# Kernel tuning notes

Measured on AMD Instinct MI355X. Metric: run time of the kernel, lower is better.

## Reference

```python
import jax, jax.numpy as jnp
import numpy as np

B, H, V, MAX_MSG_LEN = 8192, 512, 512, 16


def _uniform(key, shape, scale):
    return jax.random.uniform(key, shape, jnp.float32, -scale, scale)


def setup_inputs() -> dict:
    key = jax.random.key(0)
    ks = jax.random.split(key, 9)
    s = 1.0 / np.sqrt(H)  # torch LSTMCell/Linear default init scale
    return {
        "encoder_hidden": jax.random.normal(ks[0], (B, H), jnp.float32),
        "encoder_cell": jax.random.normal(ks[1], (B, H), jnp.float32),
        "W_ih": _uniform(ks[2], (4 * H, V), s),   # LSTMCell input weights (i,f,g,o)
        "W_hh": _uniform(ks[3], (4 * H, H), s),   # LSTMCell hidden weights
        "b_ih": _uniform(ks[4], (4 * H,), s),
        "b_hh": _uniform(ks[5], (4 * H,), s),
        "W_out": _uniform(ks[6], (V, H), s),      # nn.Linear(hidden, io_size)
        "b_out": _uniform(ks[7], (V,), s),
        "init_input": jnp.zeros((1, V), jnp.float32),  # nn.Parameter zeros
    }


def reference(encoder_hidden, encoder_cell, W_ih, W_hh, b_ih, b_hh, W_out, b_out, init_input):
    batch = encoder_hidden.shape[0]
    x0 = jnp.broadcast_to(init_input, (batch, init_input.shape[1]))

    def step(carry, _):
        x, h, c, m, lp = carry
        # torch LSTMCell: gates ordered (i, f, g, o)
        gates = x @ W_ih.T + b_ih + h @ W_hh.T + b_hh
        i, f, g, o = jnp.split(gates, 4, axis=-1)
        c = jax.nn.sigmoid(f) * c + jax.nn.sigmoid(i) * jnp.tanh(g)
        h = jax.nn.sigmoid(o) * jnp.tanh(c)
        probs = jax.nn.softmax(h @ W_out.T + b_out, axis=1)  # [B, V]
        # eval path: one-hot of argmax
        predict = jax.nn.one_hot(jnp.argmax(probs, axis=1), probs.shape[1], dtype=probs.dtype)
        lp = lp + jnp.log((probs * predict).sum(axis=1)) * m
        new_m = m * (1.0 - predict[:, -1])  # last vocab index acts as EOS
        return (predict, h, c, new_m, lp), (predict, m)

    carry0 = (x0, encoder_hidden, encoder_cell,
              jnp.ones((batch,), jnp.float32), jnp.zeros((batch,), jnp.float32))
    (_, _, _, _, log_probs), (message, masks) = jax.lax.scan(step, carry0, None, length=MAX_MSG_LEN)
    # message: [L, B, V]; mask stacked as [L, 1, B] like torch.stack of [1, B] rows
    return message, masks[:, None, :], log_probs
```

## Files before the change

kernel.cpp:

```cpp
#include <hip/hip_runtime.h>
#include <math.h>

#define Bsz 8192
#define Hd  512
#define Vd  512
#define Ld  16
#define G4  2048
#define NSLAB 16

using int4v  = __attribute__((ext_vector_type(4))) int;

__device__ __forceinline__ float sigm_f(float x){
  return __builtin_amdgcn_rcpf(1.0f + __expf(-x));
}
__device__ __forceinline__ float tanh_f(float x){
  return 1.0f - 2.0f * __builtin_amdgcn_rcpf(1.0f + __expf(2.0f * x));
}

__device__ __forceinline__ void i16split(float x, float S, signed char& a, signed char& b){
  int q = (int)rintf(x * S);
  q = min(max(q, -32640), 32639);
  const int ah = (q + 128) >> 8;
  a = (signed char)ah;
  b = (signed char)(q - (ah << 8));
}

__device__ __forceinline__ void gl_lds16(const void* g, void* l){
  __builtin_amdgcn_global_load_lds((const __attribute__((address_space(1))) void*)g,
                                   (__attribute__((address_space(3))) void*)l, 16, 0, 0);
}

#define PHASE_SYNC(N) asm volatile("s_waitcnt vmcnt(" #N ")\n\ts_barrier" ::: "memory")
#define LDS_SYNC() asm volatile("s_waitcnt lgkmcnt(0)\n\ts_barrier" ::: "memory")

#define C1I (65536.0f / (524288.0f * 32767.0f))
#define C2I (  256.0f / (524288.0f * 32767.0f))
#define C1E (65536.0f / (524288.0f * 4096.0f))
#define C2E (  256.0f / (524288.0f * 4096.0f))

#define MFMA3Q(g,bt) \
  acc1[g][bt] = __builtin_amdgcn_mfma_i32_16x16x64_i8(wA[g], hf[bt], acc1[g][bt], 0,0,0); \
  acc2[g][bt] = __builtin_amdgcn_mfma_i32_16x16x64_i8(wA[g], lf[bt], acc2[g][bt], 0,0,0); \
  acc2[g][bt] = __builtin_amdgcn_mfma_i32_16x16x64_i8(wB[g], hf[bt], acc2[g][bt], 0,0,0);

__device__ __forceinline__ int xcd_tau(int nwg_div8){
  const int lin  = blockIdx.y * gridDim.x + blockIdx.x;
  const int xcd  = lin & 7;
  const int slot = lin >> 3;
  return xcd * nwg_div8 + slot;
}

__global__ __launch_bounds__(256) void k_transpose(const float* __restrict__ in,
                                                   float* __restrict__ out){
  __shared__ float tile[32][33];
  const int tx = threadIdx.x, ty = threadIdx.y;
  const int v0 = blockIdx.x * 32, n0 = blockIdx.y * 32;
#pragma unroll
  for(int i=0;i<4;i++)
    tile[ty+i*8][tx] = in[(size_t)(n0+ty+i*8)*Vd + v0+tx];
  __syncthreads();
#pragma unroll
  for(int i=0;i<4;i++)
    out[(size_t)(v0+ty+i*8)*G4 + n0+tx] = tile[tx][ty+i*8];
}

__global__ __launch_bounds__(256) void k_split_i8(const float* __restrict__ src,
                                                  signed char* __restrict__ pa,
                                                  signed char* __restrict__ pb,
                                                  float S, int n){
  const int i = blockIdx.x*256 + threadIdx.x;
  if(i < n){
    signed char a, b;
    i16split(src[i], S, a, b);
    pa[i] = a; pb[i] = b;
  }
}

template<bool FIRST>
__global__ __launch_bounds__(512, 2) void k_lstm8(
    const signed char* __restrict__ hA, const signed char* __restrict__ hB,
    const float* __restrict__ cin,
    signed char* __restrict__ hoA, signed char* __restrict__ hoB,
    float* __restrict__ cout,
    const signed char* __restrict__ WA, const signed char* __restrict__ WB,
    const float* __restrict__ WihT, const float* __restrict__ bih,
    const float* __restrict__ bhh,
    const float* __restrict__ statM, const float* __restrict__ statS,
    const int* __restrict__ statI,
    float* __restrict__ msg, float* __restrict__ masks_out,
    float* __restrict__ lp_out, float* __restrict__ lpbuf,
    float* __restrict__ mbuf, int prev)
{
  __shared__ unsigned char lds[2][49152];
  __shared__ int gIs[256];
  const int tid = threadIdx.x;
  const int wave = tid >> 6, lane = tid & 63;
  const int tau = xcd_tau(64);
  const int mb = (tau >> 4) * 256;
  const int jb = (tau & 15) * 32;
  const int wjj = wave >> 2;
  const int wbb = wave & 3;
  const int j_wave = wjj * 16;
  const int b_wave = wbb * 64;
  const int fr = lane & 15, q = lane >> 4;
  const int lr = lane >> 2, jj = lane & 3;

  auto stW = [&](int k0, int bsel){
    unsigned char* Wa = lds[bsel];
    unsigned char* Wb = lds[bsel] + 8192;
    const int s = wave;
    const int r = s*16 + lr;
    const int j = jj ^ ((r >> 1) & 3);
    const size_t ka = (size_t)k0 + j*16;
    const size_t wrow = (size_t)((r >> 5)*Hd + jb + (r & 31));
    gl_lds16(WA + wrow*Hd + ka, &Wa[s*1024]);
    gl_lds16(WB + wrow*Hd + ka, &Wb[s*1024]);
  };
  auto stH = [&](int k0, int bsel, int half){
    unsigned char* Ha = lds[bsel] + 16384;
    unsigned char* Hb = lds[bsel] + 32768;
    const int s = (wave >> 1)*4 + half*2 + (wave & 1);
    const int r = s*16 + lr;
    const int j = jj ^ ((r >> 1) & 3);
    const size_t ka = (size_t)k0 + j*16;
    gl_lds16(hA + (size_t)(mb + r)*Hd + ka, &Ha[s*1024]);
    gl_lds16(hB + (size_t)(mb + r)*Hd + ka, &Hb[s*1024]);
  };

  stW(0, 0); stH(0, 0, 0); stH(0, 0, 1);

  int xid[4] = {0,0,0,0};
  if(!FIRST){
    if(tid < 256){
      const int row = mb + tid;
      float gm = statM[row]; int gi = statI[row];
#pragma unroll
      for(int s=1;s<NSLAB;s++){
        const float m = statM[(size_t)s*Bsz + row];
        if(m > gm){ gm = m; gi = statI[(size_t)s*Bsz + row]; }
      }
      if(jb == 0){
        float tot = 0.0f;
#pragma unroll
        for(int s=0;s<NSLAB;s++)
          tot += statS[(size_t)s*Bsz + row] * __expf(statM[(size_t)s*Bsz + row] - gm);
        const float logp = -__logf(tot);
        const float mo  = (prev == 0) ? 1.0f : mbuf[row];
        const float lpo = (prev == 0) ? 0.0f : lpbuf[row];
        const float lpn = lpo + logp * mo;
        masks_out[(size_t)prev * Bsz + row] = mo;
        lp_out[row] = lpn;
        lpbuf[row]  = lpn;
        mbuf[row]   = mo * ((gi == Vd-1) ? 0.0f : 1.0f);
      }
      gIs[tid] = gi;
    }
    LDS_SYNC();

    {
      const int r  = tid >> 1;
      const int c0 = jb + (tid & 1) * 16;
      const int gi = gIs[r];
      float* mrow = msg + ((size_t)prev * Bsz + mb + r) * Vd;
#pragma unroll
      for(int i=0;i<4;i++){
        const int c = c0 + i*4;
        float4 v;
        v.x = (c   == gi) ? 1.0f : 0.0f;
        v.y = (c+1 == gi) ? 1.0f : 0.0f;
        v.z = (c+2 == gi) ? 1.0f : 0.0f;
        v.w = (c+3 == gi) ? 1.0f : 0.0f;
        *(float4*)&mrow[c] = v;
      }
    }
#pragma unroll
    for(int bt=0;bt<4;bt++)
      xid[bt] = gIs[b_wave + bt*16 + fr];
  }

  int4v acc1[4][4], acc2[4][4];
#pragma unroll
  for(int g=0;g<4;g++)
#pragma unroll
    for(int bt=0;bt<4;bt++){
      acc1[g][bt] = (int4v){0,0,0,0};
      acc2[g][bt] = (int4v){0,0,0,0};
    }

  int4v wA[4], wB[4], hf[4], lf[4];
  for(int t=0; t<8; t++){
    const int cur = t & 1, nxt = cur ^ 1;
    const int kn = ((t+1) & 7) * 64;
    const unsigned char* Wa = lds[cur];
    const unsigned char* Wb = lds[cur] + 8192;
    const unsigned char* Ha = lds[cur] + 16384;
    const unsigned char* Hb = lds[cur] + 32768;

    PHASE_SYNC(2);
#pragma unroll
    for(int g=0;g<2;g++){
      const int r = g*32 + j_wave + fr;
      const int off = r*64 + ((q ^ ((r >> 1) & 3)) << 4);
      wA[g] = *(const int4v*)&Wa[off];
      wB[g] = *(const int4v*)&Wb[off];
    }
#pragma unroll
    for(int bt=0;bt<2;bt++){
      const int r = b_wave + bt*16 + fr;
      const int off = r*64 + ((q ^ ((r >> 1) & 3)) << 4);
      hf[bt] = *(const int4v*)&Ha[off];
      lf[bt] = *(const int4v*)&Hb[off];
    }
    stW(kn, nxt);
    __builtin_amdgcn_s_setprio(1);
#pragma unroll
    for(int g=0;g<2;g++)
#pragma unroll
      for(int bt=0;bt<2;bt++){ MFMA3Q(g,bt) }
    __builtin_amdgcn_s_setprio(0);

#pragma unroll
    for(int g=2;g<4;g++){
      const int r = g*32 + j_wave + fr;
      const int off = r*64 + ((q ^ ((r >> 1) & 3)) << 4);
      wA[g] = *(const int4v*)&Wa[off];
      wB[g] = *(const int4v*)&Wb[off];
    }
    stH(kn, nxt, 0);
    __builtin_amdgcn_s_setprio(1);
#pragma unroll
    for(int g=2;g<4;g++)
#pragma unroll
      for(int bt=0;bt<2;bt++){ MFMA3Q(g,bt) }
    __builtin_amdgcn_s_setprio(0);

    PHASE_SYNC(4);
#pragma unroll
    for(int bt=2;bt<4;bt++){
      const int r = b_wave + bt*16 + fr;
      const int off = r*64 + ((q ^ ((r >> 1) & 3)) << 4);
      hf[bt] = *(const int4v*)&Ha[off];
      lf[bt] = *(const int4v*)&Hb[off];
    }
    stH(kn, nxt, 1);
    __builtin_amdgcn_s_setprio(1);
#pragma unroll
    for(int g=0;g<2;g++)
#pragma unroll
      for(int bt=2;bt<4;bt++){ MFMA3Q(g,bt) }
    __builtin_amdgcn_s_setprio(0);

    __builtin_amdgcn_s_setprio(1);
#pragma unroll
    for(int g=2;g<4;g++)
#pragma unroll
      for(int bt=2;bt<4;bt++){ MFMA3Q(g,bt) }
    __builtin_amdgcn_s_setprio(0);
  }

  const float c1 = FIRST ? C1E : C1I;
  const float c2 = FIRST ? C2E : C2I;
  const int j0 = jb + j_wave + q*4;
  float bsum[4][4];
#pragma unroll
  for(int g=0;g<4;g++){
    float4 a = *(const float4*)&bih[g*Hd + j0];
    float4 b = *(const float4*)&bhh[g*Hd + j0];
    bsum[g][0]=a.x+b.x; bsum[g][1]=a.y+b.y; bsum[g][2]=a.z+b.z; bsum[g][3]=a.w+b.w;
  }
#pragma unroll
  for(int bt=0;bt<4;bt++){
    const int b = mb + b_wave + bt*16 + fr;
    const size_t idx = (size_t)b*Hd + j0;
    float gv[4][4];
#pragma unroll
    for(int g=0;g<4;g++)
#pragma unroll
      for(int r=0;r<4;r++)
        gv[g][r] = fmaf(c1, (float)acc1[g][bt][r],
                   fmaf(c2, (float)acc2[g][bt][r], bsum[g][r]));
    if(!FIRST){
      const float* grow = WihT + (size_t)xid[bt]*G4 + j0;
#pragma unroll
      for(int g=0;g<4;g++){
        float4 x = *(const float4*)&grow[g*Hd];
        gv[g][0]+=x.x; gv[g][1]+=x.y; gv[g][2]+=x.z; gv[g][3]+=x.w;
      }
    }
    float co[4];
    *(float4*)co = *(const float4*)&cin[idx];
    float cn[4];
    signed char a4[4], b4[4];
#pragma unroll
    for(int r=0;r<4;r++){
      const float I = sigm_f(gv[0][r]);
      const float F = sigm_f(gv[1][r]);
      const float G = tanh_f(gv[2][r]);
      const float O = sigm_f(gv[3][r]);
      cn[r] = F*co[r] + I*G;
      const float hn = O*tanh_f(cn[r]);
      i16split(hn, 32767.0f, a4[r], b4[r]);
    }
    *(float4*)&cout[idx] = *(float4*)cn;
    *(char4*)&hoA[idx] = *(char4*)a4;
    *(char4*)&hoB[idx] = *(char4*)b4;
  }
}

__global__ __launch_bounds__(512, 2) void k_logits8(
    const signed char* __restrict__ hA, const signed char* __restrict__ hB,
    const signed char* __restrict__ WoA, const signed char* __restrict__ WoB,
    const float* __restrict__ bout,
    float* __restrict__ statM, float* __restrict__ statS, int* __restrict__ statI)
{
  __shared__ unsigned char lds[2][40960];
  const int tid = threadIdx.x;
  const int wave = tid >> 6, lane = tid & 63;
  const int tau = xcd_tau(32);
  const int mb = (tau >> 3) * 256;
  const int vb = (tau & 7) * 64;
  const int wv = wave >> 2;
  const int wm = wave & 3;
  const int n_wave = wv * 32;
  const int m_wave = wm * 64;
  const int fr = lane & 15, q = lane >> 4;
  const int lr = lane >> 2, jj = lane & 3;

  auto stA = [&](int k0, int bsel){
    unsigned char* Ha = lds[bsel];
    unsigned char* Hb = lds[bsel] + 16384;
    unsigned char* Wp = lds[bsel] + 32768;
    {
      const int s = (wave >> 1)*4 + (wave & 1);
      const int r = s*16 + lr;
      const int j = jj ^ ((r >> 1) & 3);
      const size_t ka = (size_t)k0 + j*16;
      gl_lds16(hA + (size_t)(mb + r)*Hd + ka, &Ha[s*1024]);
      gl_lds16(hB + (size_t)(mb + r)*Hd + ka, &Hb[s*1024]);
    }
    {
      const int pl = wave >> 2;
      const int s  = wave & 3;
      const int r = s*16 + lr;
      const int j = jj ^ ((r >> 1) & 3);
      const size_t ka = (size_t)k0 + j*16;
      const signed char* src = pl ? WoB : WoA;
      gl_lds16(src + (size_t)(vb + r)*Hd + ka, &Wp[pl*4096 + s*1024]);
    }
  };
  auto stB = [&](int k0, int bsel){
    unsigned char* Ha = lds[bsel];
    unsigned char* Hb = lds[bsel] + 16384;
    const int s = (wave >> 1)*4 + 2 + (wave & 1);
    const int r = s*16 + lr;
    const int j = jj ^ ((r >> 1) & 3);
    const size_t ka = (size_t)k0 + j*16;
    gl_lds16(hA + (size_t)(mb + r)*Hd + ka, &Ha[s*1024]);
    gl_lds16(hB + (size_t)(mb + r)*Hd + ka, &Hb[s*1024]);
  };

  stA(0, 0); stB(0, 0);

  int4v acc1[2][4], acc2[2][4];
#pragma unroll
  for(int nt=0;nt<2;nt++)
#pragma unroll
    for(int mt=0;mt<4;mt++){
      acc1[nt][mt] = (int4v){0,0,0,0};
      acc2[nt][mt] = (int4v){0,0,0,0};
    }

  int4v ah[4], al[4], bh[2], bl[2];
  for(int t=0; t<8; t++){
    const int cur = t & 1, nxt = cur ^ 1;
    const int kn = ((t+1) & 7) * 64;
    const unsigned char* Ha = lds[cur];
    const unsigned char* Hb = lds[cur] + 16384;
    const unsigned char* Wa = lds[cur] + 32768;
    const unsigned char* Wb = lds[cur] + 36864;

    PHASE_SYNC(2);
#pragma unroll
    for(int nt=0;nt<2;nt++){
      const int r = n_wave + nt*16 + fr;
      const int off = r*64 + ((q ^ ((r >> 1) & 3)) << 4);
      bh[nt] = *(const int4v*)&Wa[off];
      bl[nt] = *(const int4v*)&Wb[off];
    }
#pragma unroll
    for(int mt=0;mt<2;mt++){
      const int r = m_wave + mt*16 + fr;
      const int off = r*64 + ((q ^ ((r >> 1) & 3)) << 4);
      ah[mt] = *(const int4v*)&Ha[off];
      al[mt] = *(const int4v*)&Hb[off];
    }
    stA(kn, nxt);
    __builtin_amdgcn_s_setprio(1);
#pragma unroll
    for(int nt=0;nt<2;nt++)
#pragma unroll
      for(int mt=0;mt<2;mt++){
        acc1[nt][mt] = __builtin_amdgcn_mfma_i32_16x16x64_i8(ah[mt], bh[nt], acc1[nt][mt], 0,0,0);
        acc2[nt][mt] = __builtin_amdgcn_mfma_i32_16x16x64_i8(ah[mt], bl[nt], acc2[nt][mt], 0,0,0);
        acc2[nt][mt] = __builtin_amdgcn_mfma_i32_16x16x64_i8(al[mt], bh[nt], acc2[nt][mt], 0,0,0);
      }
    __builtin_amdgcn_s_setprio(0);

    PHASE_SYNC(3);
#pragma unroll
    for(int mt=2;mt<4;mt++){
      const int r = m_wave + mt*16 + fr;
      const int off = r*64 + ((q ^ ((r >> 1) & 3)) << 4);
      ah[mt] = *(const int4v*)&Ha[off];
      al[mt] = *(const int4v*)&Hb[off];
    }
    stB(kn, nxt);
    __builtin_amdgcn_s_setprio(1);
#pragma unroll
    for(int nt=0;nt<2;nt++)
#pragma unroll
      for(int mt=2;mt<4;mt++){
        acc1[nt][mt] = __builtin_amdgcn_mfma_i32_16x16x64_i8(ah[mt], bh[nt], acc1[nt][mt], 0,0,0);
        acc2[nt][mt] = __builtin_amdgcn_mfma_i32_16x16x64_i8(ah[mt], bl[nt], acc2[nt][mt], 0,0,0);
        acc2[nt][mt] = __builtin_amdgcn_mfma_i32_16x16x64_i8(al[mt], bh[nt], acc2[nt][mt], 0,0,0);
      }
    __builtin_amdgcn_s_setprio(0);
  }

  const int slab = (vb >> 5) + wv;
  float bo[2];
  int vv[2];
#pragma unroll
  for(int nt=0;nt<2;nt++){
    vv[nt] = vb + n_wave + nt*16 + fr;
    bo[nt] = bout[vv[nt]];
  }
#pragma unroll
  for(int mt=0;mt<4;mt++){
#pragma unroll
    for(int reg=0;reg<4;reg++){
      float lg[2];
#pragma unroll
      for(int nt=0;nt<2;nt++)
        lg[nt] = fmaf(C1I, (float)acc1[nt][mt][reg],
                 fmaf(C2I, (float)acc2[nt][mt][reg], bo[nt]));
      float vmax = lg[0];
      int   imax = vv[0];
      if(lg[1] > vmax || (lg[1] == vmax && vv[1] < imax)){ vmax = lg[1]; imax = vv[1]; }
#pragma unroll
      for(int off=1; off<16; off<<=1){
        const float vo = __shfl_xor(vmax, off);
        const int   io = __shfl_xor(imax, off);
        if(vo > vmax || (vo == vmax && io < imax)){ vmax = vo; imax = io; }
      }
      float s = __expf(lg[0] - vmax) + __expf(lg[1] - vmax);
#pragma unroll
      for(int off=1; off<16; off<<=1) s += __shfl_xor(s, off);
      if(fr == 0){
        const int m = mb + m_wave + mt*16 + q*4 + reg;
        statM[(size_t)slab*Bsz + m] = vmax;
        statS[(size_t)slab*Bsz + m] = s;
        statI[(size_t)slab*Bsz + m] = imax;
      }
    }
  }
}

__global__ __launch_bounds__(256) void k_merge(
    const float* __restrict__ statM, const float* __restrict__ statS,
    const int* __restrict__ statI,
    float* __restrict__ msg, float* __restrict__ masks_out,
    float* __restrict__ lp_out, float* __restrict__ lpbuf,
    float* __restrict__ mbuf, int step)
{
  __shared__ int gI[32];
  const int tid = threadIdx.x;
  const int mb = blockIdx.x * 32;

  if(tid < 32){
    const int row = mb + tid;
    float gm = statM[row]; int gi = statI[row];
#pragma unroll
    for(int s=1;s<NSLAB;s++){
      const float m = statM[(size_t)s*Bsz + row];
      if(m > gm){ gm = m; gi = statI[(size_t)s*Bsz + row]; }
    }
    float tot = 0.0f;
#pragma unroll
    for(int s=0;s<NSLAB;s++)
      tot += statS[(size_t)s*Bsz + row] * __expf(statM[(size_t)s*Bsz + row] - gm);
    const float logp = -__logf(tot);
    const float mo  = mbuf[row];
    const float lpn = lpbuf[row] + logp * mo;
    masks_out[(size_t)step * Bsz + row] = mo;
    lp_out[row] = lpn;
    gI[tid] = gi;
  }
  __syncthreads();

  const int r  = tid >> 3;
  const int c8 = tid & 7;
  const int gi = gI[r];
  float* mrow = msg + ((size_t)step * Bsz + mb + r) * Vd;
#pragma unroll
  for(int i=0;i<16;i++){
    const int c = (i*8 + c8) * 4;
    float4 v;
    v.x = (c   == gi) ? 1.0f : 0.0f;
    v.y = (c+1 == gi) ? 1.0f : 0.0f;
    v.z = (c+2 == gi) ? 1.0f : 0.0f;
    v.w = (c+3 == gi) ? 1.0f : 0.0f;
    *(float4*)&mrow[c] = v;
  }
}

extern "C" void kernel_launch(void* const* d_in, const int* in_sizes, int n_in,
                              void* d_out, int out_size, void* d_ws, size_t ws_size,
                              hipStream_t stream) {
  const float* enc_h = (const float*)d_in[0];
  const float* enc_c = (const float*)d_in[1];
  const float* Wih   = (const float*)d_in[2];
  const float* Whh   = (const float*)d_in[3];
  const float* bih   = (const float*)d_in[4];
  const float* bhh   = (const float*)d_in[5];
  const float* Wout  = (const float*)d_in[6];
  const float* bout  = (const float*)d_in[7];

  float* out_msg   = (float*)d_out;
  float* out_masks = out_msg + (size_t)Ld * Bsz * Vd;
  float* out_lp    = out_masks + (size_t)Ld * Bsz;

  char* ws = (char*)d_ws;
  float* WihT  = (float*)ws;          ws += (size_t)Vd * G4 * 4;
  signed char* WhhA = (signed char*)ws; ws += (size_t)G4 * Hd;
  signed char* WhhB = (signed char*)ws; ws += (size_t)G4 * Hd;
  signed char* WoA  = (signed char*)ws; ws += (size_t)Vd * Hd;
  signed char* WoB  = (signed char*)ws; ws += (size_t)Vd * Hd;
  signed char* encA = (signed char*)ws; ws += (size_t)Bsz * Hd;
  signed char* encB = (signed char*)ws; ws += (size_t)Bsz * Hd;
  signed char* ha0  = (signed char*)ws; ws += (size_t)Bsz * Hd;
  signed char* hb0  = (signed char*)ws; ws += (size_t)Bsz * Hd;
  signed char* ha1  = (signed char*)ws; ws += (size_t)Bsz * Hd;
  signed char* hb1  = (signed char*)ws; ws += (size_t)Bsz * Hd;
  float* cbuf   = (float*)ws;  ws += (size_t)Bsz * Hd * 4;
  float* statM  = (float*)ws;  ws += (size_t)NSLAB * Bsz * 4;
  float* statS  = (float*)ws;  ws += (size_t)NSLAB * Bsz * 4;
  int*   statI  = (int*)ws;    ws += (size_t)NSLAB * Bsz * 4;
  float* lpbuf  = (float*)ws;  ws += (size_t)Bsz * 4;
  float* mbuf   = (float*)ws;  ws += (size_t)Bsz * 4;

  k_transpose<<<dim3(Vd/32, G4/32), dim3(32,8), 0, stream>>>(Wih, WihT);
  k_split_i8<<<(G4*Hd+255)/256, 256, 0, stream>>>(Whh, WhhA, WhhB, 524288.0f, G4*Hd);
  k_split_i8<<<(Vd*Hd+255)/256, 256, 0, stream>>>(Wout, WoA, WoB, 524288.0f, Vd*Hd);
  k_split_i8<<<(Bsz*Hd+255)/256, 256, 0, stream>>>(enc_h, encA, encB, 4096.0f, Bsz*Hd);

  for(int t=0; t<Ld; t++){
    signed char* haOut = (t & 1) ? ha1 : ha0;
    signed char* hbOut = (t & 1) ? hb1 : hb0;
    const signed char* haIn = (t & 1) ? ha0 : ha1;
    const signed char* hbIn = (t & 1) ? hb0 : hb1;

    if(t == 0){
      k_lstm8<true><<<dim3(Bsz/256, Hd/32), 512, 0, stream>>>(
          encA, encB, enc_c, haOut, hbOut, cbuf, WhhA, WhhB, WihT, bih, bhh,
          nullptr, nullptr, nullptr, nullptr, nullptr, nullptr, nullptr, nullptr, 0);
    } else {
      k_lstm8<false><<<dim3(Bsz/256, Hd/32), 512, 0, stream>>>(
          haIn, hbIn, cbuf, haOut, hbOut, cbuf, WhhA, WhhB, WihT, bih, bhh,
          statM, statS, statI, out_msg, out_masks, out_lp, lpbuf, mbuf, t-1);
    }
    k_logits8<<<dim3(Bsz/256, Vd/64), 512, 0, stream>>>(
        haOut, hbOut, WoA, WoB, bout, statM, statS, statI);
  }
  k_merge<<<Bsz/32, 256, 0, stream>>>(statM, statS, statI,
                                      out_msg, out_masks, out_lp,
                                      lpbuf, mbuf, Ld-1);
}
```

Before: 1.235 ms.

## Fuse LSTM step, output logits and argmax merge into one per-step kernel

Replaces the separate LSTM-gate, logits and merge kernels with a single kernel per timestep. Each block owns 32 batch rows and loops over all gate-weight chunks and then all output-weight chunks, keeping the new hidden state in LDS so the logits GEMM reads it directly. Softmax stats and argmax are reduced inside the block, which removes the slab statistics buffers and the extra launches. Gate weights and biases are interleaved per hidden unit and the cell state is stored transposed. The cost is that every block streams the full weight matrices, so weight traffic rises sharply and batch-tile reuse is much lower than the previous 256-row tiles.

```diff
diff --git a/kernel.cpp b/kernel.cpp
--- a/kernel.cpp
+++ b/kernel.cpp
@@ -6,9 +6,9 @@
 #define Vd  512
 #define Ld  16
 #define G4  2048
-#define NSLAB 16
-
-using int4v  = __attribute__((ext_vector_type(4))) int;
+#define BM  32
+
+using int4v = __attribute__((ext_vector_type(4))) int;
 
 __device__ __forceinline__ float sigm_f(float x){
   return __builtin_amdgcn_rcpf(1.0f + __expf(-x));
@@ -30,28 +30,13 @@
                                    (__attribute__((address_space(3))) void*)l, 16, 0, 0);
 }
 
-#define PHASE_SYNC(N) asm volatile("s_waitcnt vmcnt(" #N ")\n\ts_barrier" ::: "memory")
-#define LDS_SYNC() asm volatile("s_waitcnt lgkmcnt(0)\n\ts_barrier" ::: "memory")
-
 #define C1I (65536.0f / (524288.0f * 32767.0f))
 #define C2I (  256.0f / (524288.0f * 32767.0f))
 #define C1E (65536.0f / (524288.0f * 4096.0f))
 #define C2E (  256.0f / (524288.0f * 4096.0f))
 
-#define MFMA3Q(g,bt) \
-  acc1[g][bt] = __builtin_amdgcn_mfma_i32_16x16x64_i8(wA[g], hf[bt], acc1[g][bt], 0,0,0); \
-  acc2[g][bt] = __builtin_amdgcn_mfma_i32_16x16x64_i8(wA[g], lf[bt], acc2[g][bt], 0,0,0); \
-  acc2[g][bt] = __builtin_amdgcn_mfma_i32_16x16x64_i8(wB[g], hf[bt], acc2[g][bt], 0,0,0);
-
-__device__ __forceinline__ int xcd_tau(int nwg_div8){
-  const int lin  = blockIdx.y * gridDim.x + blockIdx.x;
-  const int xcd  = lin & 7;
-  const int slot = lin >> 3;
-  return xcd * nwg_div8 + slot;
-}
-
-__global__ __launch_bounds__(256) void k_transpose(const float* __restrict__ in,
-                                                   float* __restrict__ out){
+__global__ __launch_bounds__(256) void k_prep_wih(const float* __restrict__ in,
+                                                  float* __restrict__ out){
   __shared__ float tile[32][33];
   const int tx = threadIdx.x, ty = threadIdx.y;
   const int v0 = blockIdx.x * 32, n0 = blockIdx.y * 32;
@@ -59,9 +44,38 @@
   for(int i=0;i<4;i++)
     tile[ty+i*8][tx] = in[(size_t)(n0+ty+i*8)*Vd + v0+tx];
   __syncthreads();
+  const int g = n0 >> 9, jb = n0 & 511;
 #pragma unroll
   for(int i=0;i<4;i++)
-    out[(size_t)(v0+ty+i*8)*G4 + n0+tx] = tile[tx][ty+i*8];
+    out[(size_t)(v0+ty+i*8)*G4 + (jb+tx)*4 + g] = tile[tx][ty+i*8];
+}
+
+__global__ __launch_bounds__(256) void k_tr_c(const float* __restrict__ in,
+                                              float* __restrict__ out){
+  __shared__ float tile[32][33];
+  const int tx = threadIdx.x, ty = threadIdx.y;
+  const int j0 = blockIdx.x * 32, b0 = blockIdx.y * 32;
+#pragma unroll
+  for(int i=0;i<4;i++)
+    tile[ty+i*8][tx] = in[(size_t)(b0+ty+i*8)*Hd + j0+tx];
+  __syncthreads();
+#pragma unroll
+  for(int i=0;i<4;i++)
+    out[(size_t)(j0+ty+i*8)*Bsz + b0+tx] = tile[tx][ty+i*8];
+}
+
+__global__ __launch_bounds__(256) void k_split_whh(const float* __restrict__ src,
+                                                   signed char* __restrict__ pa,
+                                                   signed char* __restrict__ pb){
+  const int i = blockIdx.x*256 + threadIdx.x;
+  if(i < G4*Hd){
+    const int in_row = i >> 9, k = i & 511;
+    const int o_row = (in_row & 511)*4 + (in_row >> 9);
+    signed char a, b;
+    i16split(src[i], 524288.0f, a, b);
+    pa[(size_t)o_row*Hd + k] = a;
+    pb[(size_t)o_row*Hd + k] = b;
+  }
 }
 
 __global__ __launch_bounds__(256) void k_split_i8(const float* __restrict__ src,
@@ -76,441 +90,260 @@
   }
 }
 
+__global__ __launch_bounds__(256) void k_prep_bias(const float* __restrict__ bih,
+                                                   const float* __restrict__ bhh,
+                                                   float* __restrict__ out){
+  const int i = blockIdx.x*256 + threadIdx.x;
+  if(i < G4)
+    out[(i & 511)*4 + (i >> 9)] = bih[i] + bhh[i];
+}
+
 template<bool FIRST>
-__global__ __launch_bounds__(512, 2) void k_lstm8(
-    const signed char* __restrict__ hA, const signed char* __restrict__ hB,
-    const float* __restrict__ cin,
-    signed char* __restrict__ hoA, signed char* __restrict__ hoB,
-    float* __restrict__ cout,
-    const signed char* __restrict__ WA, const signed char* __restrict__ WB,
-    const float* __restrict__ WihT, const float* __restrict__ bih,
-    const float* __restrict__ bhh,
-    const float* __restrict__ statM, const float* __restrict__ statS,
-    const int* __restrict__ statI,
-    float* __restrict__ msg, float* __restrict__ masks_out,
-    float* __restrict__ lp_out, float* __restrict__ lpbuf,
-    float* __restrict__ mbuf, int prev)
+__global__ __launch_bounds__(512, 2) void k_step(
+    const signed char* __restrict__ hinA, const signed char* __restrict__ hinB,
+    signed char* __restrict__ hA, signed char* __restrict__ hB,
+    float* __restrict__ cT,
+    const signed char* __restrict__ WgA, const signed char* __restrict__ WgB,
+    const signed char* __restrict__ WoA, const signed char* __restrict__ WoB,
+    const float* __restrict__ WihTi, const float* __restrict__ bsum,
+    const float* __restrict__ bout,
+    int* __restrict__ gIdx, float* __restrict__ lpbuf, float* __restrict__ mbuf,
+    float* __restrict__ out_msg, float* __restrict__ out_masks,
+    float* __restrict__ out_lp, int t)
 {
-  __shared__ unsigned char lds[2][49152];
-  __shared__ int gIs[256];
+  __shared__ signed char hin[2][16384];
+  __shared__ signed char hout[2][16384];
+  __shared__ signed char wbuf[2][2][16384];
+  __shared__ float sM[8][32], sS[8][32];
+  __shared__ int   sI[8][32], gIsh[32], gFin[32];
+
   const int tid = threadIdx.x;
   const int wave = tid >> 6, lane = tid & 63;
-  const int tau = xcd_tau(64);
-  const int mb = (tau >> 4) * 256;
-  const int jb = (tau & 15) * 32;
-  const int wjj = wave >> 2;
-  const int wbb = wave & 3;
-  const int j_wave = wjj * 16;
-  const int b_wave = wbb * 64;
+  const int mb = blockIdx.x * BM;
   const int fr = lane & 15, q = lane >> 4;
   const int lr = lane >> 2, jj = lane & 3;
 
-  auto stW = [&](int k0, int bsel){
-    unsigned char* Wa = lds[bsel];
-    unsigned char* Wb = lds[bsel] + 8192;
-    const int s = wave;
-    const int r = s*16 + lr;
-    const int j = jj ^ ((r >> 1) & 3);
-    const size_t ka = (size_t)k0 + j*16;
-    const size_t wrow = (size_t)((r >> 5)*Hd + jb + (r & 31));
-    gl_lds16(WA + wrow*Hd + ka, &Wa[s*1024]);
-    gl_lds16(WB + wrow*Hd + ka, &Wb[s*1024]);
+  auto stage_hin = [&](){
+#pragma unroll
+    for(int p=0;p<4;p++){
+      const int s = wave*4 + p;
+      const int plane = s >> 4, sl = s & 15;
+      const int row = mb + (sl & 1)*16 + lr;
+      const int k = (sl >> 1)*64 + (jj ^ ((lr >> 1) & 3))*16;
+      const signed char* src = plane ? hinB : hinA;
+      gl_lds16(src + (size_t)row*Hd + k, &hin[plane][sl*1024]);
+    }
   };
-  auto stH = [&](int k0, int bsel, int half){
-    unsigned char* Ha = lds[bsel] + 16384;
-    unsigned char* Hb = lds[bsel] + 32768;
-    const int s = (wave >> 1)*4 + half*2 + (wave & 1);
-    const int r = s*16 + lr;
-    const int j = jj ^ ((r >> 1) & 3);
-    const size_t ka = (size_t)k0 + j*16;
-    gl_lds16(hA + (size_t)(mb + r)*Hd + ka, &Ha[s*1024]);
-    gl_lds16(hB + (size_t)(mb + r)*Hd + ka, &Hb[s*1024]);
+  auto stage_w = [&](const signed char* A, const signed char* B,
+                     int rowbase, int kc, int buf){
+#pragma unroll
+    for(int p=0;p<4;p++){
+      const int s = wave*4 + p;
+      const int plane = s >> 4, srow = s & 15;
+      const int row = rowbase + srow*16 + lr;
+      const int k = kc*64 + (jj ^ ((lr >> 1) & 3))*16;
+      const signed char* src = plane ? B : A;
+      gl_lds16(src + (size_t)row*Hd + k, &wbuf[buf][plane][srow*1024]);
+    }
   };
-
-  stW(0, 0); stH(0, 0, 0); stH(0, 0, 1);
-
-  int xid[4] = {0,0,0,0};
-  if(!FIRST){
-    if(tid < 256){
-      const int row = mb + tid;
-      float gm = statM[row]; int gi = statI[row];
-#pragma unroll
-      for(int s=1;s<NSLAB;s++){
-        const float m = statM[(size_t)s*Bsz + row];
-        if(m > gm){ gm = m; gi = statI[(size_t)s*Bsz + row]; }
-      }
-      if(jb == 0){
-        float tot = 0.0f;
-#pragma unroll
-        for(int s=0;s<NSLAB;s++)
-          tot += statS[(size_t)s*Bsz + row] * __expf(statM[(size_t)s*Bsz + row] - gm);
-        const float logp = -__logf(tot);
-        const float mo  = (prev == 0) ? 1.0f : mbuf[row];
-        const float lpo = (prev == 0) ? 0.0f : lpbuf[row];
-        const float lpn = lpo + logp * mo;
-        masks_out[(size_t)prev * Bsz + row] = mo;
-        lp_out[row] = lpn;
-        lpbuf[row]  = lpn;
-        mbuf[row]   = mo * ((gi == Vd-1) ? 0.0f : 1.0f);
-      }
-      gIs[tid] = gi;
-    }
-    LDS_SYNC();
-
-    {
-      const int r  = tid >> 1;
-      const int c0 = jb + (tid & 1) * 16;
-      const int gi = gIs[r];
-      float* mrow = msg + ((size_t)prev * Bsz + mb + r) * Vd;
-#pragma unroll
-      for(int i=0;i<4;i++){
-        const int c = c0 + i*4;
-        float4 v;
-        v.x = (c   == gi) ? 1.0f : 0.0f;
-        v.y = (c+1 == gi) ? 1.0f : 0.0f;
-        v.z = (c+2 == gi) ? 1.0f : 0.0f;
-        v.w = (c+3 == gi) ? 1.0f : 0.0f;
-        *(float4*)&mrow[c] = v;
-      }
-    }
-#pragma unroll
-    for(int bt=0;bt<4;bt++)
-      xid[bt] = gIs[b_wave + bt*16 + fr];
-  }
-
-  int4v acc1[4][4], acc2[4][4];
-#pragma unroll
-  for(int g=0;g<4;g++)
-#pragma unroll
-    for(int bt=0;bt<4;bt++){
-      acc1[g][bt] = (int4v){0,0,0,0};
-      acc2[g][bt] = (int4v){0,0,0,0};
-    }
-
-  int4v wA[4], wB[4], hf[4], lf[4];
-  for(int t=0; t<8; t++){
-    const int cur = t & 1, nxt = cur ^ 1;
-    const int kn = ((t+1) & 7) * 64;
-    const unsigned char* Wa = lds[cur];
-    const unsigned char* Wb = lds[cur] + 8192;
-    const unsigned char* Ha = lds[cur] + 16384;
-    const unsigned char* Hb = lds[cur] + 32768;
-
-    PHASE_SYNC(2);
-#pragma unroll
-    for(int g=0;g<2;g++){
-      const int r = g*32 + j_wave + fr;
-      const int off = r*64 + ((q ^ ((r >> 1) & 3)) << 4);
-      wA[g] = *(const int4v*)&Wa[off];
-      wB[g] = *(const int4v*)&Wb[off];
-    }
-#pragma unroll
-    for(int bt=0;bt<2;bt++){
-      const int r = b_wave + bt*16 + fr;
-      const int off = r*64 + ((q ^ ((r >> 1) & 3)) << 4);
-      hf[bt] = *(const int4v*)&Ha[off];
-      lf[bt] = *(const int4v*)&Hb[off];
-    }
-    stW(kn, nxt);
-    __builtin_amdgcn_s_setprio(1);
-#pragma unroll
-    for(int g=0;g<2;g++)
-#pragma unroll
-      for(int bt=0;bt<2;bt++){ MFMA3Q(g,bt) }
-    __builtin_amdgcn_s_setprio(0);
-
-#pragma unroll
-    for(int g=2;g<4;g++){
-      const int r = g*32 + j_wave + fr;
-      const int off = r*64 + ((q ^ ((r >> 1) & 3)) << 4);
-      wA[g] = *(const int4v*)&Wa[off];
-      wB[g] = *(const int4v*)&Wb[off];
-    }
-    stH(kn, nxt, 0);
-    __builtin_amdgcn_s_setprio(1);
-#pragma unroll
-    for(int g=2;g<4;g++)
-#pragma unroll
-      for(int bt=0;bt<2;bt++){ MFMA3Q(g,bt) }
-    __builtin_amdgcn_s_setprio(0);
-
-    PHASE_SYNC(4);
-#pragma unroll
-    for(int bt=2;bt<4;bt++){
-      const int r = b_wave + bt*16 + fr;
-      const int off = r*64 + ((q ^ ((r >> 1) & 3)) << 4);
-      hf[bt] = *(const int4v*)&Ha[off];
-      lf[bt] = *(const int4v*)&Hb[off];
-    }
-    stH(kn, nxt, 1);
-    __builtin_amdgcn_s_setprio(1);
-#pragma unroll
-    for(int g=0;g<2;g++)
-#pragma unroll
-      for(int bt=2;bt<4;bt++){ MFMA3Q(g,bt) }
-    __builtin_amdgcn_s_setprio(0);
-
-    __builtin_amdgcn_s_setprio(1);
-#pragma unroll
-    for(int g=2;g<4;g++)
-#pragma unroll
-      for(int bt=2;bt<4;bt++){ MFMA3Q(g,bt) }
-    __builtin_amdgcn_s_setprio(0);
-  }
+  auto stage_lin = [&](int s){
+    if(s < 64) stage_w(WgA, WgB, (s >> 3)*256, s & 7, s & 1);
+    else       stage_w(WoA, WoB, ((s-64) >> 3)*256, s & 7, s & 1);
+  };
+
+  stage_hin();
+  stage_lin(0);
+  if(!FIRST){ if(tid < 32) gIsh[tid] = gIdx[mb + tid]; }
 
   const float c1 = FIRST ? C1E : C1I;
   const float c2 = FIRST ? C2E : C2I;
-  const int j0 = jb + j_wave + q*4;
-  float bsum[4][4];
-#pragma unroll
-  for(int g=0;g<4;g++){
-    float4 a = *(const float4*)&bih[g*Hd + j0];
-    float4 b = *(const float4*)&bhh[g*Hd + j0];
-    bsum[g][0]=a.x+b.x; bsum[g][1]=a.y+b.y; bsum[g][2]=a.z+b.z; bsum[g][3]=a.w+b.w;
-  }
-#pragma unroll
-  for(int bt=0;bt<4;bt++){
-    const int b = mb + b_wave + bt*16 + fr;
-    const size_t idx = (size_t)b*Hd + j0;
-    float gv[4][4];
-#pragma unroll
-    for(int g=0;g<4;g++)
-#pragma unroll
-      for(int r=0;r<4;r++)
-        gv[g][r] = fmaf(c1, (float)acc1[g][bt][r],
-                   fmaf(c2, (float)acc2[g][bt][r], bsum[g][r]));
-    if(!FIRST){
-      const float* grow = WihT + (size_t)xid[bt]*G4 + j0;
-#pragma unroll
-      for(int g=0;g<4;g++){
-        float4 x = *(const float4*)&grow[g*Hd];
-        gv[g][0]+=x.x; gv[g][1]+=x.y; gv[g][2]+=x.z; gv[g][3]+=x.w;
+
+  float vm[2] = {-1e30f, -1e30f}, vs[2] = {0.0f, 0.0f};
+  int   vi[2] = {0, 0};
+
+  int4v acc1[2][2], acc2[2][2];
+#pragma unroll
+  for(int mt=0;mt<2;mt++)
+#pragma unroll
+    for(int n=0;n<2;n++){
+      acc1[mt][n] = (int4v){0,0,0,0};
+      acc2[mt][n] = (int4v){0,0,0,0};
+    }
+
+  for(int s=0; s<80; s++){
+    __syncthreads();
+    if(s+1 < 80) stage_lin(s+1);
+
+    if(s == 64){
+#pragma unroll
+      for(int p=0;p<4;p++){
+        const int l = p*512 + tid;
+        const int plane = l >> 10, li = l & 1023;
+        const int sl = li >> 6, rr = (li >> 2) & 15, jq = li & 3;
+        int4v v = *(const int4v*)&hout[plane][li*16];
+        const int row = mb + (sl & 1)*16 + rr;
+        const int k = (sl >> 1)*64 + (jq ^ ((rr >> 1) & 3))*16;
+        signed char* dst = plane ? hB : hA;
+        *(int4v*)&dst[(size_t)row*Hd + k] = v;
       }
     }
-    float co[4];
-    *(float4*)co = *(const float4*)&cin[idx];
-    float cn[4];
-    signed char a4[4], b4[4];
-#pragma unroll
-    for(int r=0;r<4;r++){
-      const float I = sigm_f(gv[0][r]);
-      const float F = sigm_f(gv[1][r]);
-      const float G = tanh_f(gv[2][r]);
-      const float O = sigm_f(gv[3][r]);
-      cn[r] = F*co[r] + I*G;
-      const float hn = O*tanh_f(cn[r]);
-      i16split(hn, 32767.0f, a4[r], b4[r]);
-    }
-    *(float4*)&cout[idx] = *(float4*)cn;
-    *(char4*)&hoA[idx] = *(char4*)a4;
-    *(char4*)&hoB[idx] = *(char4*)b4;
-  }
-}
-
-__global__ __launch_bounds__(512, 2) void k_logits8(
-    const signed char* __restrict__ hA, const signed char* __restrict__ hB,
-    const signed char* __restrict__ WoA, const signed char* __restrict__ WoB,
-    const float* __restrict__ bout,
-    float* __restrict__ statM, float* __restrict__ statS, int* __restrict__ statI)
-{
-  __shared__ unsigned char lds[2][40960];
-  const int tid = threadIdx.x;
-  const int wave = tid >> 6, lane = tid & 63;
-  const int tau = xcd_tau(32);
-  const int mb = (tau >> 3) * 256;
-  const int vb = (tau & 7) * 64;
-  const int wv = wave >> 2;
-  const int wm = wave & 3;
-  const int n_wave = wv * 32;
-  const int m_wave = wm * 64;
-  const int fr = lane & 15, q = lane >> 4;
-  const int lr = lane >> 2, jj = lane & 3;
-
-  auto stA = [&](int k0, int bsel){
-    unsigned char* Ha = lds[bsel];
-    unsigned char* Hb = lds[bsel] + 16384;
-    unsigned char* Wp = lds[bsel] + 32768;
-    {
-      const int s = (wave >> 1)*4 + (wave & 1);
-      const int r = s*16 + lr;
-      const int j = jj ^ ((r >> 1) & 3);
-      const size_t ka = (size_t)k0 + j*16;
-      gl_lds16(hA + (size_t)(mb + r)*Hd + ka, &Ha[s*1024]);
-      gl_lds16(hB + (size_t)(mb + r)*Hd + ka, &Hb[s*1024]);
-    }
-    {
-      const int pl = wave >> 2;
-      const int s  = wave & 3;
-      const int r = s*16 + lr;
-      const int j = jj ^ ((r >> 1) & 3);
-      const size_t ka = (size_t)k0 + j*16;
-      const signed char* src = pl ? WoB : WoA;
-      gl_lds16(src + (size_t)(vb + r)*Hd + ka, &Wp[pl*4096 + s*1024]);
-    }
-  };
-  auto stB = [&](int k0, int bsel){
-    unsigned char* Ha = lds[bsel];
-    unsigned char* Hb = lds[bsel] + 16384;
-    const int s = (wave >> 1)*4 + 2 + (wave & 1);
-    const int r = s*16 + lr;
-    const int j = jj ^ ((r >> 1) & 3);
-    const size_t ka = (size_t)k0 + j*16;
-    gl_lds16(hA + (size_t)(mb + r)*Hd + ka, &Ha[s*1024]);
-    gl_lds16(hB + (size_t)(mb + r)*Hd + ka, &Hb[s*1024]);
-  };
-
-  stA(0, 0); stB(0, 0);
-
-  int4v acc1[2][4], acc2[2][4];
-#pragma unroll
-  for(int nt=0;nt<2;nt++)
-#pragma unroll
-    for(int mt=0;mt<4;mt++){
-      acc1[nt][mt] = (int4v){0,0,0,0};
-      acc2[nt][mt] = (int4v){0,0,0,0};
-    }
-
-  int4v ah[4], al[4], bh[2], bl[2];
-  for(int t=0; t<8; t++){
-    const int cur = t & 1, nxt = cur ^ 1;
-    const int kn = ((t+1) & 7) * 64;
-    const unsigned char* Ha = lds[cur];
-    const unsigned char* Hb = lds[cur] + 16384;
-    const unsigned char* Wa = lds[cur] + 32768;
-    const unsigned char* Wb = lds[cur] + 36864;
-
-    PHASE_SYNC(2);
-#pragma unroll
-    for(int nt=0;nt<2;nt++){
-      const int r = n_wave + nt*16 + fr;
-      const int off = r*64 + ((q ^ ((r >> 1) & 3)) << 4);
-      bh[nt] = *(const int4v*)&Wa[off];
-      bl[nt] = *(const int4v*)&Wb[off];
-    }
+
+    const int kc = s & 7;
+    const signed char* Wa = wbuf[s&1][0];
+    const signed char* Wb = wbuf[s&1][1];
+    const signed char* Ha = (s < 64) ? hin[0] : hout[0];
+    const signed char* Hb = (s < 64) ? hin[1] : hout[1];
+
+    int4v wAv[2], wBv[2], hf[2], lf[2];
 #pragma unroll
     for(int mt=0;mt<2;mt++){
-      const int r = m_wave + mt*16 + fr;
-      const int off = r*64 + ((q ^ ((r >> 1) & 3)) << 4);
-      ah[mt] = *(const int4v*)&Ha[off];
-      al[mt] = *(const int4v*)&Hb[off];
-    }
-    stA(kn, nxt);
-    __builtin_amdgcn_s_setprio(1);
-#pragma unroll
-    for(int nt=0;nt<2;nt++)
-#pragma unroll
-      for(int mt=0;mt<2;mt++){
-        acc1[nt][mt] = __builtin_amdgcn_mfma_i32_16x16x64_i8(ah[mt], bh[nt], acc1[nt][mt], 0,0,0);
-        acc2[nt][mt] = __builtin_amdgcn_mfma_i32_16x16x64_i8(ah[mt], bl[nt], acc2[nt][mt], 0,0,0);
-        acc2[nt][mt] = __builtin_amdgcn_mfma_i32_16x16x64_i8(al[mt], bh[nt], acc2[nt][mt], 0,0,0);
+      const int off = (wave*2 + mt)*1024 + fr*64 + ((q ^ ((fr >> 1) & 3)) << 4);
+      wAv[mt] = *(const int4v*)&Wa[off];
+      wBv[mt] = *(const int4v*)&Wb[off];
+    }
+#pragma unroll
+    for(int n=0;n<2;n++){
+      const int off = (kc*2 + n)*1024 + fr*64 + ((q ^ ((fr >> 1) & 3)) << 4);
+      hf[n] = *(const int4v*)&Ha[off];
+      lf[n] = *(const int4v*)&Hb[off];
+    }
+#pragma unroll
+    for(int mt=0;mt<2;mt++)
+#pragma unroll
+      for(int n=0;n<2;n++){
+        acc1[mt][n] = __builtin_amdgcn_mfma_i32_16x16x64_i8(wAv[mt], hf[n], acc1[mt][n],0,0,0);
+        acc2[mt][n] = __builtin_amdgcn_mfma_i32_16x16x64_i8(wAv[mt], lf[n], acc2[mt][n],0,0,0);
+        acc2[mt][n] = __builtin_amdgcn_mfma_i32_16x16x64_i8(wBv[mt], hf[n], acc2[mt][n],0,0,0);
       }
-    __builtin_amdgcn_s_setprio(0);
-
-    PHASE_SYNC(3);
-#pragma unroll
-    for(int mt=2;mt<4;mt++){
-      const int r = m_wave + mt*16 + fr;
-      const int off = r*64 + ((q ^ ((r >> 1) & 3)) << 4);
-      ah[mt] = *(const int4v*)&Ha[off];
-      al[mt] = *(const int4v*)&Hb[off];
-    }
-    stB(kn, nxt);
-    __builtin_amdgcn_s_setprio(1);
-#pragma unroll
-    for(int nt=0;nt<2;nt++)
-#pragma unroll
-      for(int mt=2;mt<4;mt++){
-        acc1[nt][mt] = __builtin_amdgcn_mfma_i32_16x16x64_i8(ah[mt], bh[nt], acc1[nt][mt], 0,0,0);
-        acc2[nt][mt] = __builtin_amdgcn_mfma_i32_16x16x64_i8(ah[mt], bl[nt], acc2[nt][mt], 0,0,0);
-        acc2[nt][mt] = __builtin_amdgcn_mfma_i32_16x16x64_i8(al[mt], bh[nt], acc2[nt][mt], 0,0,0);
+
+    if(kc == 7){
+      if(s < 64){
+        const int nc = s >> 3;
+#pragma unroll
+        for(int mt=0;mt<2;mt++){
+          const int j = nc*64 + (wave*2 + mt)*4 + q;
+          const float4 bs = *(const float4*)&bsum[j*4];
+#pragma unroll
+          for(int n=0;n<2;n++){
+            const int rl = n*16 + fr;
+            const int row = mb + rl;
+            float base[4] = {bs.x, bs.y, bs.z, bs.w};
+            if(!FIRST){
+              const float4 wx = *(const float4*)&WihTi[(size_t)gIsh[rl]*G4 + j*4];
+              base[0]+=wx.x; base[1]+=wx.y; base[2]+=wx.z; base[3]+=wx.w;
+            }
+            float g4[4];
+#pragma unroll
+            for(int r=0;r<4;r++)
+              g4[r] = fmaf(c1, (float)acc1[mt][n][r],
+                      fmaf(c2, (float)acc2[mt][n][r], base[r]));
+            const float I = sigm_f(g4[0]);
+            const float F = sigm_f(g4[1]);
+            const float G = tanh_f(g4[2]);
+            const float O = sigm_f(g4[3]);
+            const size_t cidx = (size_t)j*Bsz + row;
+            const float cn = F*cT[cidx] + I*G;
+            cT[cidx] = cn;
+            const float hn = O*tanh_f(cn);
+            signed char a, b;
+            i16split(hn, 32767.0f, a, b);
+            const int rr = rl & 15;
+            const int addr = ((j >> 6)*2 + (rl >> 4))*1024 + rr*64
+                           + ((((j >> 4) & 3) ^ ((rr >> 1) & 3)) << 4) + (j & 15);
+            hout[0][addr] = a;
+            hout[1][addr] = b;
+            acc1[mt][n] = (int4v){0,0,0,0};
+            acc2[mt][n] = (int4v){0,0,0,0};
+          }
+        }
+      } else {
+        const int vc = (s - 64) >> 3;
+#pragma unroll
+        for(int mt=0;mt<2;mt++){
+          const int vb4 = vc*256 + (wave*2 + mt)*16 + q*4;
+          const float4 bo = *(const float4*)&bout[vb4];
+          const float bo4[4] = {bo.x, bo.y, bo.z, bo.w};
+#pragma unroll
+          for(int n=0;n<2;n++){
+#pragma unroll
+            for(int r=0;r<4;r++){
+              const float lg = fmaf(C1I, (float)acc1[mt][n][r],
+                               fmaf(C2I, (float)acc2[mt][n][r], bo4[r]));
+              if(lg > vm[n]){
+                vs[n] = vs[n]*__expf(vm[n] - lg) + 1.0f;
+                vm[n] = lg; vi[n] = vb4 + r;
+              } else {
+                vs[n] += __expf(lg - vm[n]);
+              }
+            }
+            acc1[mt][n] = (int4v){0,0,0,0};
+            acc2[mt][n] = (int4v){0,0,0,0};
+          }
+        }
       }
-    __builtin_amdgcn_s_setprio(0);
-  }
-
-  const int slab = (vb >> 5) + wv;
-  float bo[2];
-  int vv[2];
-#pragma unroll
-  for(int nt=0;nt<2;nt++){
-    vv[nt] = vb + n_wave + nt*16 + fr;
-    bo[nt] = bout[vv[nt]];
-  }
-#pragma unroll
-  for(int mt=0;mt<4;mt++){
-#pragma unroll
-    for(int reg=0;reg<4;reg++){
-      float lg[2];
-#pragma unroll
-      for(int nt=0;nt<2;nt++)
-        lg[nt] = fmaf(C1I, (float)acc1[nt][mt][reg],
-                 fmaf(C2I, (float)acc2[nt][mt][reg], bo[nt]));
-      float vmax = lg[0];
-      int   imax = vv[0];
-      if(lg[1] > vmax || (lg[1] == vmax && vv[1] < imax)){ vmax = lg[1]; imax = vv[1]; }
-#pragma unroll
-      for(int off=1; off<16; off<<=1){
-        const float vo = __shfl_xor(vmax, off);
-        const int   io = __shfl_xor(imax, off);
-        if(vo > vmax || (vo == vmax && io < imax)){ vmax = vo; imax = io; }
-      }
-      float s = __expf(lg[0] - vmax) + __expf(lg[1] - vmax);
-#pragma unroll
-      for(int off=1; off<16; off<<=1) s += __shfl_xor(s, off);
-      if(fr == 0){
-        const int m = mb + m_wave + mt*16 + q*4 + reg;
-        statM[(size_t)slab*Bsz + m] = vmax;
-        statS[(size_t)slab*Bsz + m] = s;
-        statI[(size_t)slab*Bsz + m] = imax;
-      }
-    }
-  }
-}
-
-__global__ __launch_bounds__(256) void k_merge(
-    const float* __restrict__ statM, const float* __restrict__ statS,
-    const int* __restrict__ statI,
-    float* __restrict__ msg, float* __restrict__ masks_out,
-    float* __restrict__ lp_out, float* __restrict__ lpbuf,
-    float* __restrict__ mbuf, int step)
-{
-  __shared__ int gI[32];
-  const int tid = threadIdx.x;
-  const int mb = blockIdx.x * 32;
+    }
+  }
+
+#pragma unroll
+  for(int n=0;n<2;n++){
+#pragma unroll
+    for(int off=16; off<64; off<<=1){
+      const float vmo = __shfl_xor(vm[n], off);
+      const float vso = __shfl_xor(vs[n], off);
+      const int   vio = __shfl_xor(vi[n], off);
+      if(vmo > vm[n]){ vs[n] = vs[n]*__expf(vm[n]-vmo) + vso; vm[n]=vmo; vi[n]=vio; }
+      else if(vmo == vm[n]){ vs[n] += vso; vi[n] = min(vi[n], vio); }
+      else vs[n] += vso*__expf(vmo - vm[n]);
+    }
+  }
+  if(lane < 16){
+#pragma unroll
+    for(int n=0;n<2;n++){
+      sM[wave][n*16+lane] = vm[n];
+      sS[wave][n*16+lane] = vs[n];
+      sI[wave][n*16+lane] = vi[n];
+    }
+  }
+  __syncthreads();
 
   if(tid < 32){
+    float M = sM[0][tid], S = sS[0][tid];
+    int   I = sI[0][tid];
+#pragma unroll
+    for(int w=1;w<8;w++){
+      const float Mo = sM[w][tid], So = sS[w][tid];
+      const int   Io = sI[w][tid];
+      if(Mo > M){ S = S*__expf(M-Mo) + So; M = Mo; I = Io; }
+      else if(Mo == M){ S += So; I = min(I, Io); }
+      else S += So*__expf(Mo - M);
+    }
+    const float logp = -__logf(S);
     const int row = mb + tid;
-    float gm = statM[row]; int gi = statI[row];
-#pragma unroll
-    for(int s=1;s<NSLAB;s++){
-      const float m = statM[(size_t)s*Bsz + row];
-      if(m > gm){ gm = m; gi = statI[(size_t)s*Bsz + row]; }
-    }
-    float tot = 0.0f;
-#pragma unroll
-    for(int s=0;s<NSLAB;s++)
-      tot += statS[(size_t)s*Bsz + row] * __expf(statM[(size_t)s*Bsz + row] - gm);
-    const float logp = -__logf(tot);
-    const float mo  = mbuf[row];
-    const float lpn = lpbuf[row] + logp * mo;
-    masks_out[(size_t)step * Bsz + row] = mo;
-    lp_out[row] = lpn;
-    gI[tid] = gi;
+    const float mo = FIRST ? 1.0f : mbuf[row];
+    const float lp = (FIRST ? 0.0f : lpbuf[row]) + logp*mo;
+    out_masks[(size_t)t*Bsz + row] = mo;
+    lpbuf[row] = lp;
+    out_lp[row] = lp;
+    mbuf[row] = mo * ((I == Vd-1) ? 0.0f : 1.0f);
+    gIdx[row] = I;
+    gFin[tid] = I;
   }
   __syncthreads();
 
-  const int r  = tid >> 3;
-  const int c8 = tid & 7;
-  const int gi = gI[r];
-  float* mrow = msg + ((size_t)step * Bsz + mb + r) * Vd;
-#pragma unroll
-  for(int i=0;i<16;i++){
-    const int c = (i*8 + c8) * 4;
-    float4 v;
-    v.x = (c   == gi) ? 1.0f : 0.0f;
-    v.y = (c+1 == gi) ? 1.0f : 0.0f;
-    v.z = (c+2 == gi) ? 1.0f : 0.0f;
-    v.w = (c+3 == gi) ? 1.0f : 0.0f;
-    *(float4*)&mrow[c] = v;
+  {
+    const int rowl = tid >> 4, c0 = (tid & 15)*32;
+    const int gi = gFin[rowl];
+    float* mrow = out_msg + ((size_t)t*Bsz + mb + rowl)*Vd;
+#pragma unroll
+    for(int i=0;i<8;i++){
+      const int c = c0 + i*4;
+      float4 v;
+      v.x = (c   == gi) ? 1.0f : 0.0f;
+      v.y = (c+1 == gi) ? 1.0f : 0.0f;
+      v.z = (c+2 == gi) ? 1.0f : 0.0f;
+      v.w = (c+3 == gi) ? 1.0f : 0.0f;
+      *(float4*)&mrow[c] = v;
+    }
   }
 }
 
@@ -531,48 +364,37 @@
   float* out_lp    = out_masks + (size_t)Ld * Bsz;
 
   char* ws = (char*)d_ws;
-  float* WihT  = (float*)ws;          ws += (size_t)Vd * G4 * 4;
-  signed char* WhhA = (signed char*)ws; ws += (size_t)G4 * Hd;
-  signed char* WhhB = (signed char*)ws; ws += (size_t)G4 * Hd;
-  signed char* WoA  = (signed char*)ws; ws += (size_t)Vd * Hd;
-  signed char* WoB  = (signed char*)ws; ws += (size_t)Vd * Hd;
+  float* WihTi = (float*)ws;            ws += (size_t)Vd * G4 * 4;
+  signed char* WgA = (signed char*)ws;  ws += (size_t)G4 * Hd;
+  signed char* WgB = (signed char*)ws;  ws += (size_t)G4 * Hd;
+  signed char* WoA = (signed char*)ws;  ws += (size_t)Vd * Hd;
+  signed char* WoB = (signed char*)ws;  ws += (size_t)Vd * Hd;
   signed char* encA = (signed char*)ws; ws += (size_t)Bsz * Hd;
   signed char* encB = (signed char*)ws; ws += (size_t)Bsz * Hd;
-  signed char* ha0  = (signed char*)ws; ws += (size_t)Bsz * Hd;
-  signed char* hb0  = (signed char*)ws; ws += (size_t)Bsz * Hd;
-  signed char* ha1  = (signed char*)ws; ws += (size_t)Bsz * Hd;
-  signed char* hb1  = (signed char*)ws; ws += (size_t)Bsz * Hd;
-  float* cbuf   = (float*)ws;  ws += (size_t)Bsz * Hd * 4;
-  float* statM  = (float*)ws;  ws += (size_t)NSLAB * Bsz * 4;
-  float* statS  = (float*)ws;  ws += (size_t)NSLAB * Bsz * 4;
-  int*   statI  = (int*)ws;    ws += (size_t)NSLAB * Bsz * 4;
-  float* lpbuf  = (float*)ws;  ws += (size_t)Bsz * 4;
-  float* mbuf   = (float*)ws;  ws += (size_t)Bsz * 4;
-
-  k_transpose<<<dim3(Vd/32, G4/32), dim3(32,8), 0, stream>>>(Wih, WihT);
-  k_split_i8<<<(G4*Hd+255)/256, 256, 0, stream>>>(Whh, WhhA, WhhB, 524288.0f, G4*Hd);
+  signed char* hA  = (signed char*)ws;  ws += (size_t)Bsz * Hd;
+  signed char* hB  = (signed char*)ws;  ws += (size_t)Bsz * Hd;
+  float* cT    = (float*)ws;            ws += (size_t)Hd * Bsz * 4;
+  float* bsum  = (float*)ws;            ws += (size_t)G4 * 4;
+  int*   gIdx  = (int*)ws;              ws += (size_t)Bsz * 4;
+  float* lpbuf = (float*)ws;            ws += (size_t)Bsz * 4;
+  float* mbuf  = (float*)ws;            ws += (size_t)Bsz * 4;
+
+  k_prep_wih<<<dim3(Vd/32, G4/32), dim3(32,8), 0, stream>>>(Wih, WihTi);
+  k_tr_c<<<dim3(Hd/32, Bsz/32), dim3(32,8), 0, stream>>>(enc_c, cT);
+  k_split_whh<<<(G4*Hd+255)/256, 256, 0, stream>>>(Whh, WgA, WgB);
   k_split_i8<<<(Vd*Hd+255)/256, 256, 0, stream>>>(Wout, WoA, WoB, 524288.0f, Vd*Hd);
   k_split_i8<<<(Bsz*Hd+255)/256, 256, 0, stream>>>(enc_h, encA, encB, 4096.0f, Bsz*Hd);
+  k_prep_bias<<<(G4+255)/256, 256, 0, stream>>>(bih, bhh, bsum);
 
   for(int t=0; t<Ld; t++){
-    signed char* haOut = (t & 1) ? ha1 : ha0;
-    signed char* hbOut = (t & 1) ? hb1 : hb0;
-    const signed char* haIn = (t & 1) ? ha0 : ha1;
-    const signed char* hbIn = (t & 1) ? hb0 : hb1;
-
     if(t == 0){
-      k_lstm8<true><<<dim3(Bsz/256, Hd/32), 512, 0, stream>>>(
-          encA, encB, enc_c, haOut, hbOut, cbuf, WhhA, WhhB, WihT, bih, bhh,
-          nullptr, nullptr, nullptr, nullptr, nullptr, nullptr, nullptr, nullptr, 0);
+      k_step<true><<<dim3(Bsz/BM), dim3(512), 0, stream>>>(
+          encA, encB, hA, hB, cT, WgA, WgB, WoA, WoB, WihTi, bsum, bout,
+          gIdx, lpbuf, mbuf, out_msg, out_masks, out_lp, 0);
     } else {
-      k_lstm8<false><<<dim3(Bsz/256, Hd/32), 512, 0, stream>>>(
-          haIn, hbIn, cbuf, haOut, hbOut, cbuf, WhhA, WhhB, WihT, bih, bhh,
-          statM, statS, statI, out_msg, out_masks, out_lp, lpbuf, mbuf, t-1);
-    }
-    k_logits8<<<dim3(Bsz/256, Vd/64), 512, 0, stream>>>(
-        haOut, hbOut, WoA, WoB, bout, statM, statS, statI);
-  }
-  k_merge<<<Bsz/32, 256, 0, stream>>>(statM, statS, statI,
-                                      out_msg, out_masks, out_lp,
-                                      lpbuf, mbuf, Ld-1);
-}
+      k_step<false><<<dim3(Bsz/BM), dim3(512), 0, stream>>>(
+          hA, hB, hA, hB, cT, WgA, WgB, WoA, WoB, WihTi, bsum, bout,
+          gIdx, lpbuf, mbuf, out_msg, out_masks, out_lp, t);
+    }
+  }
+}
```

Result: slower. 1.898 ms (+53.7%).
